# Kernel optimization log

Measured on AMD Instinct MI355X. Metric: run time of the kernel, lower is better.

Reference implementation:

```python
import jax, jax.numpy as jnp
import numpy as np

MARGIN = 0.3
PD_EPS = 1e-6  # torch F.pairwise_distance adds eps to the difference


def setup_inputs() -> dict:
    key = jax.random.key(0)
    k1, k2 = jax.random.split(key)
    B, D, NUM_CLASSES = 8192, 256, 8
    embeddings = jax.random.normal(k1, (B, D), dtype=jnp.float32)
    labels = jax.random.randint(k2, (B,), 0, NUM_CLASSES, dtype=jnp.int64)
    return {"embeddings": embeddings, "labels": labels}


def _pairwise_euclidean(x):
    # cdist(x, x, p=2) via the Gram trick; clamp tiny negatives before sqrt
    sq = jnp.sum(x * x, axis=1)  # [B]
    d2 = sq[:, None] + sq[None, :] - 2.0 * (x @ x.T)
    return jnp.sqrt(jnp.maximum(d2, 0.0))


def reference(embeddings, labels):
    B = embeddings.shape[0]
    D = _pairwise_euclidean(embeddings)  # [B, B]

    eq = labels[:, None] == labels[None, :]
    eye = jnp.eye(B, dtype=bool)
    pos_mask = eq & ~eye          # same label, not self
    neg_mask = ~eq                # different label

    # hard mining: per anchor, farthest positive and closest negative
    pos_idx = jnp.argmax(jnp.where(pos_mask, D, -jnp.inf), axis=1)  # [B]
    neg_idx = jnp.argmin(jnp.where(neg_mask, D, jnp.inf), axis=1)   # [B]
    valid = pos_mask.any(axis=1) & neg_mask.any(axis=1)             # [B]

    # recompute triplet distances like F.pairwise_distance (eps on the diff)
    pos_dist = jnp.linalg.norm(embeddings - embeddings[pos_idx] + PD_EPS, axis=1)
    neg_dist = jnp.linalg.norm(embeddings - embeddings[neg_idx] + PD_EPS, axis=1)

    per_anchor = jax.nn.relu(pos_dist - neg_dist + MARGIN)
    n_valid = jnp.maximum(valid.sum(), 1)
    loss = jnp.sum(jnp.where(valid, per_anchor, 0.0)) / n_valid.astype(per_anchor.dtype)
    return loss
```

## Files before the change

### kernel.cpp

```cpp
#include <hip/hip_runtime.h>
#include <math.h>


typedef __attribute__((ext_vector_type(8))) short short8;
typedef __attribute__((ext_vector_type(4))) float floatx4;

#define B_N 8192
#define D_K 256

__device__ __forceinline__ unsigned short f2bf_rne(float f) {
  unsigned u = __float_as_uint(f);
  u += 0x7FFFu + ((u >> 16) & 1u);
  return (unsigned short)(u >> 16);
}

__device__ __forceinline__ void gl_lds16(const unsigned short* g, unsigned short* l) {
  __builtin_amdgcn_global_load_lds(
      (const __attribute__((address_space(1))) unsigned int*)g,
      (__attribute__((address_space(3))) unsigned int*)l, 16, 0, 0);
}

#define DPP_SHR(x, CTRL) \
  ((unsigned)__builtin_amdgcn_update_dpp((int)(x), (int)(x), (CTRL), 0xF, 0xF, false))

__global__ void k_hist(const int* __restrict__ lab, int* __restrict__ chunkhist,
                       float* __restrict__ sum, int* __restrict__ cnt,
                       int* __restrict__ done) {
  __shared__ int h[8];
  const int tid = threadIdx.x, b = blockIdx.x;
  if (tid < 8) h[tid] = 0;
  __syncthreads();
  atomicAdd(&h[lab[b * 256 + tid] & 7], 1);
  __syncthreads();
  if (tid < 8) chunkhist[b * 8 + tid] = h[tid];
  if (b == 0 && tid == 0) { *sum = 0.f; *cnt = 0; *done = 0; }
}

__global__ void k_perm(const int* __restrict__ lab, const int* __restrict__ chunkhist,
                       int* __restrict__ perm, int* __restrict__ labp) {
  __shared__ int ch[256];
  __shared__ int base[8];
  __shared__ int wcnt[4][8];
  const int tid = threadIdx.x, b = blockIdx.x;
  ch[tid] = chunkhist[tid];
  __syncthreads();
  if (tid < 8) {
    const int c = tid;
    int acc = 0;
    for (int cc = 0; cc < c; ++cc)
      for (int k = 0; k < 32; ++k) acc += ch[k * 8 + cc];
    for (int k = 0; k < b; ++k) acc += ch[k * 8 + c];
    base[c] = acc;
  }
  const int i    = b * 256 + tid;
  const int myc  = lab[i] & 7;
  const int lane = tid & 63, w = tid >> 6;
  unsigned long long bal[8];
#pragma unroll
  for (int c = 0; c < 8; ++c) bal[c] = __ballot(myc == c);
  if (lane == 0) {
#pragma unroll
    for (int c = 0; c < 8; ++c) wcnt[w][c] = (int)__popcll(bal[c]);
  }
  __syncthreads();
  int rank = (int)__popcll(bal[myc] & ((1ull << lane) - 1ull));
  for (int ww = 0; ww < w; ++ww) rank += wcnt[ww][myc];
  const int pos = base[myc] + rank;
  perm[pos] = i;
  labp[pos] = myc;
}

__global__ void k_split(const float* __restrict__ x, const int* __restrict__ perm,
                        unsigned short* __restrict__ xhf,
                        float* __restrict__ sqq) {
  __shared__ float sw[64];
  const int tid  = threadIdx.x;
  const int lane = tid & 63;
  const int w    = tid >> 6;
  const int b    = blockIdx.x;
  const int m    = lane & 15;
  const int quad = lane >> 4;
  const int row  = b * 16 + m;
  const int rsrc = perm[row];

  float s = 0.f;
#pragma unroll
  for (int h = 0; h < 2; ++h) {
    int tk = w + h * 4;
    int kk = tk * 32 + quad * 8;
    float4 f0 = *reinterpret_cast<const float4*>(x + (size_t)rsrc * D_K + kk);
    float4 f1 = *reinterpret_cast<const float4*>(x + (size_t)rsrc * D_K + kk + 4);
    s += f0.x * f0.x + f0.y * f0.y + f0.z * f0.z + f0.w * f0.w;
    s += f1.x * f1.x + f1.y * f1.y + f1.z * f1.z + f1.w * f1.w;
    ushort4 lo, hi;
    lo.x = f2bf_rne(f0.x); lo.y = f2bf_rne(f0.y); lo.z = f2bf_rne(f0.z); lo.w = f2bf_rne(f0.w);
    hi.x = f2bf_rne(f1.x); hi.y = f2bf_rne(f1.y); hi.z = f2bf_rne(f1.z); hi.w = f2bf_rne(f1.w);
    size_t o = ((size_t)b * 8 + tk) * 512 + lane * 8;
    *reinterpret_cast<ushort4*>(xhf + o)     = lo;
    *reinterpret_cast<ushort4*>(xhf + o + 4) = hi;
  }
  s += __shfl_xor(s, 16);
  s += __shfl_xor(s, 32);
  if (quad == 0) sw[w * 16 + m] = s;
  __syncthreads();
  if (tid < 16) {
    int i = b * 16 + tid;
    float t = sw[tid] + sw[16 + tid] + sw[32 + tid] + sw[48 + tid];
    sqq[i] = fmaf(t, 128.f, 262144.f);
  }
}

template <int MODE>
__device__ __forceinline__ void mine_tail(
    const floatx4* acc, const int* __restrict__ labp, const float* __restrict__ sqq,
    int i0, int bi, int bj, int w, int lane,
    unsigned* jbp, unsigned* jbn, unsigned* ibp, unsigned* ibn,
    unsigned* __restrict__ ppart, unsigned* __restrict__ npart) {
  const int wj = w & 1;
  const int quad = lane >> 4, l15 = lane & 15;

  float sqi[16];
#pragma unroll
  for (int r = 0; r < 16; ++r)
    sqi[r] = sqq[i0 + (r >> 2) * 16 + quad * 4 + (r & 3)];

  unsigned long long lip = 0ull;
  if (MODE == 2) {
#pragma unroll
    for (int r = 0; r < 16; ++r) {
      int ir = i0 + (r >> 2) * 16 + quad * 4 + (r & 3);
      lip |= (unsigned long long)((unsigned)labp[ir] & 0xFu) << (r * 4);
    }
  }

  unsigned pkey[16], nkey[16];
#pragma unroll
  for (int r = 0; r < 16; ++r) { pkey[r] = 0u; nkey[r] = 0xFFFFFFFFu; }

#pragma unroll
  for (int nt = 0; nt < 4; ++nt) {
    const int      j  = bj * 128 + wj * 64 + nt * 16 + l15;
    const float    sj = sqq[j];
    const unsigned jl = (MODE == 2) ? ((unsigned)labp[j] & 0xFu) : 0u;
    unsigned jp = 0u, jn = 0xFFFFFFFFu;
#pragma unroll
    for (int r = 0; r < 16; ++r) {
      float dot = acc[(r >> 2) * 4 + nt][r & 3];
      int   ir  = i0 + (r >> 2) * 16 + quad * 4 + (r & 3);
      unsigned keyi = ((unsigned)fmaf(-256.f, dot, sj) << 13) | (unsigned)j;
      unsigned keyj = ((unsigned)fmaf(-256.f, dot, sqi[r]) << 13) | (unsigned)ir;
      if (MODE == 2) {
        bool eq = (jl == (unsigned)((lip >> (r * 4)) & 0xFull));
        unsigned pci = eq ? keyi : 0u;
        unsigned nci = eq ? 0xFFFFFFFFu : keyi;
        pkey[r] = pkey[r] > pci ? pkey[r] : pci;
        nkey[r] = nkey[r] < nci ? nkey[r] : nci;
        unsigned pcj = eq ? keyj : 0u;
        unsigned ncj = eq ? 0xFFFFFFFFu : keyj;
        jp = jp > pcj ? jp : pcj;
        jn = jn < ncj ? jn : ncj;
      } else if (MODE == 1) {
        pkey[r] = pkey[r] > keyi ? pkey[r] : keyi;
        jp = jp > keyj ? jp : keyj;
      } else {
        nkey[r] = nkey[r] < keyi ? nkey[r] : keyi;
        jn = jn < keyj ? jn : keyj;
      }
    }
#pragma unroll
    for (int m = 16; m < 64; m <<= 1) {
      if (MODE != 0) { unsigned op = (unsigned)__shfl_xor((int)jp, m); jp = jp > op ? jp : op; }
      if (MODE != 1) { unsigned on = (unsigned)__shfl_xor((int)jn, m); jn = jn < on ? jn : on; }
    }
    if (quad == 0) {
      jbp[w * 64 + nt * 16 + l15] = (MODE == 0) ? 0u : jp;
      jbn[w * 64 + nt * 16 + l15] = (MODE == 1) ? 0xFFFFFFFFu : jn;
    }
  }

#pragma unroll
  for (int r = 0; r < 16; ++r) {
    if (MODE != 0) { unsigned tp = DPP_SHR(pkey[r], 0x118); pkey[r] = pkey[r] > tp ? pkey[r] : tp; }
    if (MODE != 1) { unsigned tn = DPP_SHR(nkey[r], 0x118); nkey[r] = nkey[r] < tn ? nkey[r] : tn; }
  }
#pragma unroll
  for (int r = 0; r < 16; ++r) {
    if (MODE != 0) { unsigned tp = DPP_SHR(pkey[r], 0x114); pkey[r] = pkey[r] > tp ? pkey[r] : tp; }
    if (MODE != 1) { unsigned tn = DPP_SHR(nkey[r], 0x114); nkey[r] = nkey[r] < tn ? nkey[r] : tn; }
  }
#pragma unroll
  for (int r = 0; r < 16; ++r) {
    if (MODE != 0) { unsigned tp = DPP_SHR(pkey[r], 0x112); pkey[r] = pkey[r] > tp ? pkey[r] : tp; }
    if (MODE != 1) { unsigned tn = DPP_SHR(nkey[r], 0x112); nkey[r] = nkey[r] < tn ? nkey[r] : tn; }
  }
#pragma unroll
  for (int r = 0; r < 16; ++r) {
    if (MODE != 0) { unsigned tp = DPP_SHR(pkey[r], 0x111); pkey[r] = pkey[r] > tp ? pkey[r] : tp; }
    if (MODE != 1) { unsigned tn = DPP_SHR(nkey[r], 0x111); nkey[r] = nkey[r] < tn ? nkey[r] : tn; }
  }
#pragma unroll
  for (int r = 0; r < 16; ++r) {
    if (l15 == 15) {
      int row = (r >> 2) * 16 + quad * 4 + (r & 3);
      ibp[w * 64 + row] = (MODE == 0) ? 0u : pkey[r];
      ibn[w * 64 + row] = (MODE == 1) ? 0xFFFFFFFFu : nkey[r];
    }
  }

  __syncthreads();
  if ((w & 1) == 0) {
    const int half = w >> 1;
    unsigned p  = ibp[(2 * half) * 64 + lane];
    unsigned p2 = ibp[(2 * half + 1) * 64 + lane];
    unsigned n  = ibn[(2 * half) * 64 + lane];
    unsigned n2 = ibn[(2 * half + 1) * 64 + lane];
    p = p > p2 ? p : p2;
    n = n < n2 ? n : n2;
    int ir = bi * 128 + half * 64 + lane;
    size_t idx = (size_t)bj * B_N + ir;
    ppart[idx] = p;
    npart[idx] = n;
  } else if (bi != bj) {
    const int jh = w >> 1;
    unsigned p  = jbp[jh * 64 + lane];
    unsigned p2 = jbp[(jh + 2) * 64 + lane];
    unsigned n  = jbn[jh * 64 + lane];
    unsigned n2 = jbn[(jh + 2) * 64 + lane];
    p = p > p2 ? p : p2;
    n = n < n2 ? n : n2;
    int j = bj * 128 + jh * 64 + lane;
    size_t idx = (size_t)bi * B_N + j;
    ppart[idx] = p;
    npart[idx] = n;
  }
}

__global__ __launch_bounds__(256, 3) void k_mine16(
    const unsigned short* __restrict__ xhf, const int* __restrict__ labp,
    const float* __restrict__ sqq,
    unsigned* __restrict__ ppart, unsigned* __restrict__ npart) {
  __shared__ unsigned short stage[2][16][512];
  __shared__ unsigned jbp[4 * 64], jbn[4 * 64];
  __shared__ unsigned ibp[4 * 64], ibn[4 * 64];

  int t  = blockIdx.x;
  int bi = (int)(64.5f - sqrtf(64.5f * 64.5f - 2.f * (float)t));
  int b0 = 64 * bi - (bi * (bi - 1)) / 2;
  if (t < b0) { bi--; b0 = 64 * bi - (bi * (bi - 1)) / 2; }
  else {
    int b1 = 64 * (bi + 1) - ((bi + 1) * bi) / 2;
    if (t >= b1) { bi++; b0 = b1; }
  }
  const int bj = bi + (t - b0);

  const int tid  = threadIdx.x;
  const int lane = tid & 63;
  const int w    = tid >> 6;
  const int wi   = w >> 1;
  const int wj   = w & 1;
  const int i0   = bi * 128 + wi * 64;

  const int la0 = labp[bi * 128];
  const int la1 = labp[bi * 128 + 127];
  const int lb0 = labp[bj * 128];
  const int lb1 = labp[bj * 128 + 127];

  const unsigned short* srcA0 = xhf + (size_t)(bi * 8 + w)     * 4096 + lane * 8;
  const unsigned short* srcA1 = xhf + (size_t)(bi * 8 + 4 + w) * 4096 + lane * 8;
  const unsigned short* srcB0 = xhf + (size_t)(bj * 8 + w)     * 4096 + lane * 8;
  const unsigned short* srcB1 = xhf + (size_t)(bj * 8 + 4 + w) * 4096 + lane * 8;

#define STAGE(bf, tk)                                             \
  do {                                                            \
    gl_lds16(srcA0 + (tk) * 512, &stage[bf][w][0]);               \
    gl_lds16(srcA1 + (tk) * 512, &stage[bf][4 + w][0]);           \
    gl_lds16(srcB0 + (tk) * 512, &stage[bf][8 + w][0]);           \
    gl_lds16(srcB1 + (tk) * 512, &stage[bf][12 + w][0]);          \
  } while (0)

  floatx4 acc[16];
#pragma unroll
  for (int q = 0; q < 16; ++q) acc[q] = (floatx4)0.f;

  STAGE(0, 0);
  __syncthreads();

  int bf = 0;
#pragma unroll
  for (int tk = 0; tk < 8; ++tk) {
    if (tk < 7) STAGE(bf ^ 1, tk + 1);
    short8 Bf[4];
#pragma unroll
    for (int nt = 0; nt < 4; ++nt)
      Bf[nt] = *reinterpret_cast<const short8*>(&stage[bf][8 + wj * 4 + nt][lane * 8]);
    short8 Af[4];
#pragma unroll
    for (int mt = 0; mt < 4; ++mt)
      Af[mt] = *reinterpret_cast<const short8*>(&stage[bf][wi * 4 + mt][lane * 8]);
#pragma unroll
    for (int mt = 0; mt < 4; ++mt)
#pragma unroll
      for (int nt = 0; nt < 4; ++nt)
        acc[mt * 4 + nt] = __builtin_amdgcn_mfma_f32_16x16x32_bf16(
            Af[mt], Bf[nt], acc[mt * 4 + nt], 0, 0, 0);
    __syncthreads();
    bf ^= 1;
  }
#undef STAGE

  if (la1 < lb0 || lb1 < la0) {
    mine_tail<0>(acc, labp, sqq, i0, bi, bj, w, lane, jbp, jbn, ibp, ibn, ppart, npart);
  } else if (la0 == lb1 && la1 == lb0) {
    mine_tail<1>(acc, labp, sqq, i0, bi, bj, w, lane, jbp, jbn, ibp, ibn, ppart, npart);
  } else {
    mine_tail<2>(acc, labp, sqq, i0, bi, bj, w, lane, jbp, jbn, ibp, ibn, ppart, npart);
  }
}

__global__ void k_finish(const float* __restrict__ x, const int* __restrict__ perm,
                         const unsigned* __restrict__ ppart,
                         const unsigned* __restrict__ npart,
                         float* __restrict__ sum, int* __restrict__ cnt,
                         int* __restrict__ done, float* __restrict__ out) {
  __shared__ unsigned spk[32], snk[32];
  __shared__ float ssum[4];
  __shared__ int   scnt[4];
  const int tid = threadIdx.x;
  const int a0  = blockIdx.x * 32;

  if (tid < 32) { spk[tid] = 0u; snk[tid] = 0xFFFFFFFFu; }
  __syncthreads();

  {
    const int a    = a0 + (tid & 31);
    const int part = tid >> 5;
    unsigned p = 0u, n = 0xFFFFFFFFu;
#pragma unroll
    for (int s = 0; s < 8; ++s) {
      size_t idx = (size_t)(part * 8 + s) * B_N + a;
      unsigned pv = ppart[idx];
      unsigned nv = npart[idx];
      p = p > pv ? p : pv;
      n = n < nv ? n : nv;
    }
    atomicMax(&spk[tid & 31], p);
    atomicMin(&snk[tid & 31], n);
  }
  __syncthreads();

  const int w = tid >> 6, lane = tid & 63;
  float lsum = 0.f; int lcnt = 0;
#pragma unroll
  for (int it = 0; it < 8; ++it) {
    int al = w * 8 + it;
    int a  = a0 + al;
    unsigned p = spk[al];
    unsigned n = snk[al];
    bool valid = (p != 0u) && (n != 0xFFFFFFFFu);
    int  pidx = valid ? (int)(p & 8191u) : 0;
    int  nidx = valid ? (int)(n & 8191u) : 0;
    int  ra = perm[a], rp = perm[pidx], rn = perm[nidx];

    float4 xa = *reinterpret_cast<const float4*>(x + (size_t)ra * D_K + lane * 4);
    float4 xp = *reinterpret_cast<const float4*>(x + (size_t)rp * D_K + lane * 4);
    float4 xn = *reinterpret_cast<const float4*>(x + (size_t)rn * D_K + lane * 4);
    float dx, sp = 0.f, sn = 0.f;
    dx = xa.x - xp.x + 1e-6f; sp = fmaf(dx, dx, sp);
    dx = xa.y - xp.y + 1e-6f; sp = fmaf(dx, dx, sp);
    dx = xa.z - xp.z + 1e-6f; sp = fmaf(dx, dx, sp);
    dx = xa.w - xp.w + 1e-6f; sp = fmaf(dx, dx, sp);
    dx = xa.x - xn.x + 1e-6f; sn = fmaf(dx, dx, sn);
    dx = xa.y - xn.y + 1e-6f; sn = fmaf(dx, dx, sn);
    dx = xa.z - xn.z + 1e-6f; sn = fmaf(dx, dx, sn);
    dx = xa.w - xn.w + 1e-6f; sn = fmaf(dx, dx, sn);
#pragma unroll
    for (int o = 32; o > 0; o >>= 1) {
      sp += __shfl_down(sp, o, 64);
      sn += __shfl_down(sn, o, 64);
    }
    if (lane == 0 && valid) {
      float per = sqrtf(sp) - sqrtf(sn) + 0.3f;
      if (per > 0.f) lsum += per;
      lcnt += 1;
    }
  }
  if (lane == 0) { ssum[w] = lsum; scnt[w] = lcnt; }
  __syncthreads();
  if (tid == 0) {
    atomicAdd(sum, ssum[0] + ssum[1] + ssum[2] + ssum[3]);
    atomicAdd(cnt, scnt[0] + scnt[1] + scnt[2] + scnt[3]);
    __threadfence();
    int prev = atomicAdd(done, 1);
    if (prev == gridDim.x - 1) {
      float s = atomicAdd(sum, 0.f);
      int   cc = atomicAdd(cnt, 0);
      if (cc < 1) cc = 1;
      out[0] = s / (float)cc;
    }
  }
}

extern "C" void kernel_launch(void* const* d_in, const int* in_sizes, int n_in,
                              void* d_out, int out_size, void* d_ws, size_t ws_size,
                              hipStream_t stream) {
  const float* x   = (const float*)d_in[0];
  const int*   lab = (const int*)d_in[1];
  float*       out = (float*)d_out;

  char* ws = (char*)d_ws;
  unsigned short* xhf = (unsigned short*)ws;
  int* perm      = (int*)(ws + (size_t)4096 * 1024);
  int* labp      = (int*)(ws + (size_t)4096 * 1024 + 32768);
  int* chunkhist = (int*)(ws + (size_t)4096 * 1024 + 65536);
  float* sqq = (float*)(ws + (size_t)4608 * 1024);
  char*  pb = ws + (size_t)4608 * 1024 + 65536;
  size_t seg = (size_t)64 * B_N * 4;
  unsigned* ppart = (unsigned*)(pb);
  unsigned* npart = (unsigned*)(pb + seg);
  float* sum  = (float*)(pb + 2 * seg);
  int*   cnt  = (int*)(sum + 1);
  int*   done = (int*)(sum + 2);

  k_hist<<<32, 256, 0, stream>>>(lab, chunkhist, sum, cnt, done);
  k_perm<<<32, 256, 0, stream>>>(lab, chunkhist, perm, labp);
  k_split<<<B_N / 16, 256, 0, stream>>>(x, perm, xhf, sqq);
  k_mine16<<<2080, 256, 0, stream>>>(xhf, labp, sqq, ppart, npart);
  k_finish<<<B_N / 32, 256, 0, stream>>>(x, perm, ppart, npart, sum, cnt, done, out);
}
```

Baseline: 114.7 us.

## Enlarge mining tile to 128x256 with 8 waves per block

Reshapes the symmetric pairwise-distance mining tile from 128x128 with 4 waves into 128x256 with 8 waves, so each loaded B panel is reused across more rows and the triangular grid shrinks from 2080 to 1056 blocks. The index mapping over the upper triangle, the partial-result layout (96 segments) and the finish kernel's reduction, which now skips segments that were never written, are rewritten to match. This adds LDS per block, raises register pressure under the new launch bounds, and makes the finish pass read a more irregular set of partials.

New measurement: 121.9 us. 6.2% more time.

```diff
diff --git a/kernel.cpp b/kernel.cpp
--- a/kernel.cpp
+++ b/kernel.cpp
@@ -116,7 +116,7 @@
     int i0, int bi, int bj, int w, int lane,
     unsigned* jbp, unsigned* jbn, unsigned* ibp, unsigned* ibn,
     unsigned* __restrict__ ppart, unsigned* __restrict__ npart) {
-  const int wj = w & 1;
+  const int wi = w >> 2, wj = w & 3;
   const int quad = lane >> 4, l15 = lane & 15;
 
   float sqi[16];
@@ -139,7 +139,7 @@
 
 #pragma unroll
   for (int nt = 0; nt < 4; ++nt) {
-    const int      j  = bj * 128 + wj * 64 + nt * 16 + l15;
+    const int      j  = bj * 256 + wj * 64 + nt * 16 + l15;
     const float    sj = sqq[j];
     const unsigned jl = (MODE == 2) ? ((unsigned)labp[j] & 0xFu) : 0u;
     unsigned jp = 0u, jn = 0xFFFFFFFFu;
@@ -208,74 +208,76 @@
   }
 
   __syncthreads();
-  if ((w & 1) == 0) {
-    const int half = w >> 1;
-    unsigned p  = ibp[(2 * half) * 64 + lane];
-    unsigned p2 = ibp[(2 * half + 1) * 64 + lane];
-    unsigned n  = ibn[(2 * half) * 64 + lane];
-    unsigned n2 = ibn[(2 * half + 1) * 64 + lane];
-    p = p > p2 ? p : p2;
-    n = n < n2 ? n : n2;
-    int ir = bi * 128 + half * 64 + lane;
+  if (wi == 0) {
+    if (bi != 2 * bj && bi != 2 * bj + 1) {
+      unsigned p  = jbp[wj * 64 + lane];
+      unsigned p2 = jbp[(4 + wj) * 64 + lane];
+      unsigned n  = jbn[wj * 64 + lane];
+      unsigned n2 = jbn[(4 + wj) * 64 + lane];
+      p = p > p2 ? p : p2;
+      n = n < n2 ? n : n2;
+      int j = bj * 256 + wj * 64 + lane;
+      size_t idx = (size_t)(32 + bi) * B_N + j;
+      ppart[idx] = p;
+      npart[idx] = n;
+    }
+  } else if (wj < 2) {
+    const int h = wj;
+    unsigned p = ibp[(4 * h) * 64 + lane];
+    unsigned n = ibn[(4 * h) * 64 + lane];
+#pragma unroll
+    for (int c = 1; c < 4; ++c) {
+      unsigned p2 = ibp[(4 * h + c) * 64 + lane];
+      unsigned n2 = ibn[(4 * h + c) * 64 + lane];
+      p = p > p2 ? p : p2;
+      n = n < n2 ? n : n2;
+    }
+    int ir = bi * 128 + h * 64 + lane;
     size_t idx = (size_t)bj * B_N + ir;
     ppart[idx] = p;
     npart[idx] = n;
-  } else if (bi != bj) {
-    const int jh = w >> 1;
-    unsigned p  = jbp[jh * 64 + lane];
-    unsigned p2 = jbp[(jh + 2) * 64 + lane];
-    unsigned n  = jbn[jh * 64 + lane];
-    unsigned n2 = jbn[(jh + 2) * 64 + lane];
-    p = p > p2 ? p : p2;
-    n = n < n2 ? n : n2;
-    int j = bj * 128 + jh * 64 + lane;
-    size_t idx = (size_t)bi * B_N + j;
-    ppart[idx] = p;
-    npart[idx] = n;
-  }
-}
-
-__global__ __launch_bounds__(256, 3) void k_mine16(
+  }
+}
+
+__global__ __launch_bounds__(512, 4) void k_mine16(
     const unsigned short* __restrict__ xhf, const int* __restrict__ labp,
     const float* __restrict__ sqq,
     unsigned* __restrict__ ppart, unsigned* __restrict__ npart) {
-  __shared__ unsigned short stage[2][16][512];
-  __shared__ unsigned jbp[4 * 64], jbn[4 * 64];
-  __shared__ unsigned ibp[4 * 64], ibn[4 * 64];
+  __shared__ unsigned short stage[2][24][512];
+  __shared__ unsigned jbp[8 * 64], jbn[8 * 64];
+  __shared__ unsigned ibp[8 * 64], ibn[8 * 64];
 
   int t  = blockIdx.x;
-  int bi = (int)(64.5f - sqrtf(64.5f * 64.5f - 2.f * (float)t));
-  int b0 = 64 * bi - (bi * (bi - 1)) / 2;
-  if (t < b0) { bi--; b0 = 64 * bi - (bi * (bi - 1)) / 2; }
+  int bj = (int)(32.5f - sqrtf(1056.25f - (float)t));
+  int b0 = bj * (65 - bj);
+  if (t < b0) { bj--; b0 = bj * (65 - bj); }
   else {
-    int b1 = 64 * (bi + 1) - ((bi + 1) * bi) / 2;
-    if (t >= b1) { bi++; b0 = b1; }
-  }
-  const int bj = bi + (t - b0);
+    int b1 = (bj + 1) * (64 - bj);
+    if (t >= b1) { bj++; b0 = b1; }
+  }
+  const int bi = 2 * bj + (t - b0);
 
   const int tid  = threadIdx.x;
   const int lane = tid & 63;
   const int w    = tid >> 6;
-  const int wi   = w >> 1;
-  const int wj   = w & 1;
+  const int wi   = w >> 2;
+  const int wj   = w & 3;
   const int i0   = bi * 128 + wi * 64;
 
   const int la0 = labp[bi * 128];
   const int la1 = labp[bi * 128 + 127];
-  const int lb0 = labp[bj * 128];
-  const int lb1 = labp[bj * 128 + 127];
-
-  const unsigned short* srcA0 = xhf + (size_t)(bi * 8 + w)     * 4096 + lane * 8;
-  const unsigned short* srcA1 = xhf + (size_t)(bi * 8 + 4 + w) * 4096 + lane * 8;
-  const unsigned short* srcB0 = xhf + (size_t)(bj * 8 + w)     * 4096 + lane * 8;
-  const unsigned short* srcB1 = xhf + (size_t)(bj * 8 + 4 + w) * 4096 + lane * 8;
+  const int lb0 = labp[bj * 256];
+  const int lb1 = labp[bj * 256 + 255];
+
+  const unsigned short* src0 = xhf + (size_t)(bi * 8 + w)       * 4096 + lane * 8;
+  const unsigned short* src1 = xhf + (size_t)(bj * 16 + w)      * 4096 + lane * 8;
+  const unsigned short* src2 = xhf + (size_t)(bj * 16 + 8 + w)  * 4096 + lane * 8;
 
 #define STAGE(bf, tk)                                             \
   do {                                                            \
-    gl_lds16(srcA0 + (tk) * 512, &stage[bf][w][0]);               \
-    gl_lds16(srcA1 + (tk) * 512, &stage[bf][4 + w][0]);           \
-    gl_lds16(srcB0 + (tk) * 512, &stage[bf][8 + w][0]);           \
-    gl_lds16(srcB1 + (tk) * 512, &stage[bf][12 + w][0]);          \
+    gl_lds16(src0 + (tk) * 512, &stage[bf][w][0]);                \
+    gl_lds16(src1 + (tk) * 512, &stage[bf][8 + w][0]);            \
+    gl_lds16(src2 + (tk) * 512, &stage[bf][16 + w][0]);           \
   } while (0)
 
   floatx4 acc[16];
@@ -285,9 +287,9 @@
   STAGE(0, 0);
   __syncthreads();
 
-  int bf = 0;
 #pragma unroll
   for (int tk = 0; tk < 8; ++tk) {
+    const int bf = tk & 1;
     if (tk < 7) STAGE(bf ^ 1, tk + 1);
     short8 Bf[4];
 #pragma unroll
@@ -304,7 +306,6 @@
         acc[mt * 4 + nt] = __builtin_amdgcn_mfma_f32_16x16x32_bf16(
             Af[mt], Bf[nt], acc[mt * 4 + nt], 0, 0, 0);
     __syncthreads();
-    bf ^= 1;
   }
 #undef STAGE
 
@@ -334,14 +335,17 @@
   {
     const int a    = a0 + (tid & 31);
     const int part = tid >> 5;
+    const int aB   = a >> 8;
+    const int jlo  = 34 + 2 * aB;
     unsigned p = 0u, n = 0xFFFFFFFFu;
-#pragma unroll
-    for (int s = 0; s < 8; ++s) {
-      size_t idx = (size_t)(part * 8 + s) * B_N + a;
-      unsigned pv = ppart[idx];
-      unsigned nv = npart[idx];
-      p = p > pv ? p : pv;
-      n = n < nv ? n : nv;
+    for (int s = part; s < 96; s += 8) {
+      if (s <= aB || s >= jlo) {
+        size_t idx = (size_t)s * B_N + a;
+        unsigned pv = ppart[idx];
+        unsigned nv = npart[idx];
+        p = p > pv ? p : pv;
+        n = n < nv ? n : nv;
+      }
     }
     atomicMax(&spk[tid & 31], p);
     atomicMin(&snk[tid & 31], n);
@@ -414,7 +418,7 @@
   int* chunkhist = (int*)(ws + (size_t)4096 * 1024 + 65536);
   float* sqq = (float*)(ws + (size_t)4608 * 1024);
   char*  pb = ws + (size_t)4608 * 1024 + 65536;
-  size_t seg = (size_t)64 * B_N * 4;
+  size_t seg = (size_t)96 * B_N * 4;
   unsigned* ppart = (unsigned*)(pb);
   unsigned* npart = (unsigned*)(pb + seg);
   float* sum  = (float*)(pb + 2 * seg);
@@ -424,6 +428,6 @@
   k_hist<<<32, 256, 0, stream>>>(lab, chunkhist, sum, cnt, done);
   k_perm<<<32, 256, 0, stream>>>(lab, chunkhist, perm, labp);
   k_split<<<B_N / 16, 256, 0, stream>>>(x, perm, xhf, sqq);
-  k_mine16<<<2080, 256, 0, stream>>>(xhf, labp, sqq, ppart, npart);
+  k_mine16<<<1056, 512, 0, stream>>>(xhf, labp, sqq, ppart, npart);
   k_finish<<<B_N / 32, 256, 0, stream>>>(x, perm, ppart, npart, sum, cnt, done, out);
 }
```
